# Performance work log

Measured on AMD Instinct MI355X. Metric: run time of the kernel, lower is better.

The kernel has to match this reference:

```python
import jax, jax.numpy as jnp
import numpy as np

DIM = 1024
NUM_EXPERTS = 8
TOP_K = 2


def setup_inputs() -> dict:
    key = jax.random.key(0)
    ks = jax.random.split(key, 7)
    s_in = 1.0 / np.sqrt(DIM)
    s_hid = 1.0 / np.sqrt(4 * DIM)
    x = jax.random.normal(ks[0], (2, 2048, DIM), dtype=jnp.float32)
    gate_w = jax.random.normal(ks[1], (DIM, NUM_EXPERTS), dtype=jnp.float32) * s_in
    gate_b = jax.random.normal(ks[2], (NUM_EXPERTS,), dtype=jnp.float32) * 0.01
    w1 = jax.random.normal(ks[3], (NUM_EXPERTS, DIM, 4 * DIM), dtype=jnp.float32) * s_in
    b1 = jax.random.normal(ks[4], (NUM_EXPERTS, 4 * DIM), dtype=jnp.float32) * 0.01
    w2 = jax.random.normal(ks[5], (NUM_EXPERTS, 4 * DIM, DIM), dtype=jnp.float32) * s_hid
    b2 = jax.random.normal(ks[6], (NUM_EXPERTS, DIM), dtype=jnp.float32) * 0.01
    return {"x": x, "gate_w": gate_w, "gate_b": gate_b, "w1": w1, "b1": b1, "w2": w2, "b2": b2}


def reference(x, gate_w, gate_b, w1, b1, w2, b2):
    # Faithful to the torch module in EVAL mode (no routing noise).
    # Quirks reproduced: (1) gather of expert inputs degenerates to flat_x
    # (all top_k copies identical); (2) softmax-normalized gates are dead code
    # (never applied); (3) the per-expert masked assignment overwrites all
    # TOP_K. Net: out = TOP_K * FFN_{max(topk_idx)}(x).
    B, N, C = x.shape
    flat_x = x.reshape(-1, C)                      # [T, C]
    logits = flat_x @ gate_w + gate_b              # [T, E]
    _, topk_idx = jax.lax.top_k(logits, TOP_K)     # [T, k]
    e_star = jnp.max(topk_idx, axis=-1)            # [T] last-overwriting expert
    out = jnp.zeros_like(flat_x)
    for i in range(NUM_EXPERTS):                   # fixed small expert loop
        h = jax.nn.gelu(flat_x @ w1[i] + b1[i], approximate=False)  # exact GELU (torch default)
        y = h @ w2[i] + b2[i]                      # [T, C]
        out = jnp.where((e_star == i)[:, None], y, out)
    return (TOP_K * out).reshape(B, N, C)
```

## Files before the change

### kernel.cpp

```cpp
#include <hip/hip_runtime.h>
#include <hip/hip_bf16.h>
#include <hip/hip_fp16.h>

#define T_TOKENS 4096
#define DIMC 1024
#define HID 4096
#define NE 8

typedef _Float16 f16;
typedef _Float16 f16x8 __attribute__((ext_vector_type(8)));
typedef _Float16 f16x4 __attribute__((ext_vector_type(4)));
typedef float f32x4 __attribute__((ext_vector_type(4)));

__device__ __forceinline__ void gload_lds16(const f16* g, f16* l) {
    __builtin_amdgcn_global_load_lds(
        (const __attribute__((address_space(1))) void*)g,
        (__attribute__((address_space(3))) void*)l, 16, 0, 0);
}

__global__ __launch_bounds__(256) void gating_kernel(
    const float* __restrict__ x, const float* __restrict__ gw,
    const float* __restrict__ gb, int* __restrict__ counts,
    int* __restrict__ list)
{
    const int wave = threadIdx.x >> 6;
    const int lane = threadIdx.x & 63;
    const int t = blockIdx.x * 4 + wave;

    const float* xr = x + (size_t)t * DIMC;
    float acc[NE];
#pragma unroll
    for (int e = 0; e < NE; ++e) acc[e] = 0.f;

    for (int i = 0; i < DIMC / 64; ++i) {
        const int k = i * 64 + lane;
        const float xv = xr[k];
        const float* g = gw + (size_t)k * NE;
#pragma unroll
        for (int e = 0; e < NE; ++e) acc[e] = fmaf(xv, g[e], acc[e]);
    }
#pragma unroll
    for (int off = 32; off >= 1; off >>= 1) {
#pragma unroll
        for (int e = 0; e < NE; ++e) acc[e] += __shfl_xor(acc[e], off, 64);
    }
    if (lane == 0) {
        float lg[NE];
#pragma unroll
        for (int e = 0; e < NE; ++e) lg[e] = acc[e] + gb[e];
        int i1 = 0; float v1 = lg[0];
#pragma unroll
        for (int e = 1; e < NE; ++e) { if (lg[e] > v1) { v1 = lg[e]; i1 = e; } }
        int i2 = -1; float v2 = -3.4e38f;
#pragma unroll
        for (int e = 0; e < NE; ++e) {
            if (e == i1) continue;
            if (lg[e] > v2) { v2 = lg[e]; i2 = e; }
        }
        const int es = (i1 > i2) ? i1 : i2;
        const int pos = atomicAdd(&counts[es], 1);
        list[es * T_TOKENS + pos] = t;
    }
}

__global__ __launch_bounds__(256) void xconvert(const float* __restrict__ x,
                                                f16* __restrict__ xh)
{
    const size_t i = ((size_t)blockIdx.x * 256 + threadIdx.x) * 8;
    const float4 a = *(const float4*)(x + i);
    const float4 b = *(const float4*)(x + i + 4);
    f16x8 v;
    v[0] = (f16)a.x; v[1] = (f16)a.y; v[2] = (f16)a.z; v[3] = (f16)a.w;
    v[4] = (f16)b.x; v[5] = (f16)b.y; v[6] = (f16)b.z; v[7] = (f16)b.w;
    *(f16x8*)(xh + i) = v;
}

__global__ __launch_bounds__(256) void wconvert(const float* __restrict__ W,
                                                f16* __restrict__ Wt,
                                                int K, int N)
{
    __shared__ f16 Lt[64 * 72];
    const int n0 = blockIdx.x * 64;
    const int k0 = blockIdx.y * 64;
    const float* Ws = W + (size_t)blockIdx.z * K * N;
    const int t = threadIdx.x;

    const int no = (t & 15) * 4;
    const int kr = t >> 4;
#pragma unroll
    for (int p = 0; p < 4; ++p) {
        const int k = kr + p * 16;
        const float4 v = *(const float4*)(Ws + (size_t)(k0 + k) * N + n0 + no);
        Lt[(no + 0) * 72 + k] = (f16)v.x;
        Lt[(no + 1) * 72 + k] = (f16)v.y;
        Lt[(no + 2) * 72 + k] = (f16)v.z;
        Lt[(no + 3) * 72 + k] = (f16)v.w;
    }
    __syncthreads();
    const int n = t >> 2;
    const int ko = (t & 3) * 16;
    const f16x8 a = *(const f16x8*)&Lt[n * 72 + ko];
    const f16x8 b = *(const f16x8*)&Lt[n * 72 + ko + 8];
    f16* dst = Wt + ((size_t)blockIdx.z * N + n0 + n) * K + k0 + ko;
    *(f16x8*)(dst) = a;
    *(f16x8*)(dst + 8) = b;
}

template <bool FIRST>
__global__ __launch_bounds__(256) void ffn_gemm4(
    const f16* __restrict__ A, const f16* __restrict__ Bt,
    const float* __restrict__ bias, const int* __restrict__ counts,
    const int* __restrict__ list, f16* __restrict__ Hout,
    float* __restrict__ pout)
{
    constexpr int KB   = FIRST ? DIMC : HID;
    constexpr int NTOT = FIRST ? HID : DIMC;

    const int e   = FIRST ? (int)blockIdx.z : (int)(blockIdx.z >> 2);
    const int ks  = FIRST ? 0 : (int)(blockIdx.z & 3);
    const int kk0 = ks * 1024;
    const int m0  = blockIdx.y * 128;
    const int n0  = blockIdx.x * 128;
    const int cnt = counts[e];
    if (m0 >= cnt) return;

    __shared__ __align__(16) f16 As[2][128 * 64];
    __shared__ __align__(16) f16 Bs[2][128 * 64];
    __shared__ int rows[128];

    const int tid = threadIdx.x;
    if (tid < 128) rows[tid] = (m0 + tid < cnt) ? list[e * T_TOKENS + m0 + tid] : -1;
    __syncthreads();

    const int lane = tid & 63;
    const int wv   = tid >> 6;
    const int wr   = wv >> 1, wc = wv & 1;

    const f16* asrc[4];
    const f16* bsrc[4];
#pragma unroll
    for (int j = 0; j < 4; ++j) {
        const int row   = wv * 32 + j * 8 + (lane >> 3);
        const int chunk = (lane & 7) ^ (row & 7);
        int tok = rows[row]; if (tok < 0) tok = 0;
        asrc[j] = A + (size_t)tok * KB + kk0 + chunk * 8;
        bsrc[j] = Bt + ((size_t)e * NTOT + n0 + row) * KB + kk0 + chunk * 8;
    }

    f32x4 acc[4][4];
#pragma unroll
    for (int mi = 0; mi < 4; ++mi)
#pragma unroll
        for (int ni = 0; ni < 4; ++ni) acc[mi][ni] = f32x4{0.f, 0.f, 0.f, 0.f};

#define STAGE(BUF, KO)                                                     \
    _Pragma("unroll")                                                      \
    for (int j = 0; j < 4; ++j) {                                          \
        gload_lds16(asrc[j] + (KO), &As[BUF][(wv * 32 + j * 8) * 64]);     \
        gload_lds16(bsrc[j] + (KO), &Bs[BUF][(wv * 32 + j * 8) * 64]);     \
    }

#define COMPUTE(BUF)                                                       \
    _Pragma("unroll")                                                      \
    for (int kh = 0; kh < 2; ++kh) {                                       \
        f16x8 af[4], bf[4];                                                \
        _Pragma("unroll")                                                  \
        for (int mi = 0; mi < 4; ++mi) {                                   \
            const int row = wr * 64 + mi * 16 + (lane & 15);               \
            const int kb  = (((lane >> 4) * 16) + kh * 64) ^ ((row & 7) << 4); \
            af[mi] = *(const f16x8*)((const char*)As[BUF] + row * 128 + kb);   \
        }                                                                  \
        _Pragma("unroll")                                                  \
        for (int ni = 0; ni < 4; ++ni) {                                   \
            const int n  = wc * 64 + ni * 16 + (lane & 15);                \
            const int kb = (((lane >> 4) * 16) + kh * 64) ^ ((n & 7) << 4);\
            bf[ni] = *(const f16x8*)((const char*)Bs[BUF] + n * 128 + kb); \
        }                                                                  \
        _Pragma("unroll")                                                  \
        for (int mi = 0; mi < 4; ++mi)                                     \
            _Pragma("unroll")                                              \
            for (int ni = 0; ni < 4; ++ni)                                 \
                acc[mi][ni] = __builtin_amdgcn_mfma_f32_16x16x32_f16(      \
                    af[mi], bf[ni], acc[mi][ni], 0, 0, 0);                 \
    }

    STAGE(0, 0);
    __syncthreads();
#pragma unroll
    for (int kt2 = 0; kt2 < 8; ++kt2) {
        STAGE(1, (2 * kt2 + 1) * 64);
        COMPUTE(0);
        __syncthreads();
        if (kt2 < 7) { STAGE(0, (2 * kt2 + 2) * 64); }
        COMPUTE(1);
        __syncthreads();
    }
#undef STAGE
#undef COMPUTE

#pragma unroll
    for (int ni = 0; ni < 4; ++ni) {
        const int gc = n0 + wc * 64 + ni * 16 + (lane & 15);
        const float bv = FIRST ? bias[(size_t)e * HID + gc]
                               : ((ks == 0) ? 2.f * bias[(size_t)e * DIMC + gc] : 0.f);
#pragma unroll
        for (int mi = 0; mi < 4; ++mi) {
#pragma unroll
            for (int r = 0; r < 4; ++r) {
                const int lrow = wr * 64 + mi * 16 + (lane >> 4) * 4 + r;
                const int tok = rows[lrow];
                if (tok < 0) continue;
                if (FIRST) {
                    const float v = acc[mi][ni][r] + bv;
                    const float g = 0.5f * v * (1.f + erff(v * 0.70710678118f));
                    Hout[(size_t)tok * HID + gc] = (f16)g;
                } else {
                    pout[((size_t)ks * T_TOKENS + tok) * DIMC + gc] =
                        2.f * acc[mi][ni][r] + bv;
                }
            }
        }
    }
}

__global__ __launch_bounds__(256) void reduce4(const float* __restrict__ p,
                                               float* __restrict__ out)
{
    constexpr size_t SL = (size_t)T_TOKENS * DIMC;
    const size_t i = ((size_t)blockIdx.x * 256 + threadIdx.x) * 4;
    const float4 a = *(const float4*)(p + i);
    const float4 b = *(const float4*)(p + SL + i);
    const float4 c = *(const float4*)(p + 2 * SL + i);
    const float4 d = *(const float4*)(p + 3 * SL + i);
    float4 s;
    s.x = a.x + b.x + c.x + d.x;
    s.y = a.y + b.y + c.y + d.y;
    s.z = a.z + b.z + c.z + d.z;
    s.w = a.w + b.w + c.w + d.w;
    *(float4*)(out + i) = s;
}

template <bool FIRST>
__global__ __launch_bounds__(256) void ffn_gemm3(
    const f16* __restrict__ A, const f16* __restrict__ Bt,
    const float* __restrict__ bias, const int* __restrict__ counts,
    const int* __restrict__ list, f16* __restrict__ Hout,
    float* __restrict__ out)
{
    constexpr int KB   = FIRST ? DIMC : HID;
    constexpr int NTOT = FIRST ? HID : DIMC;
    constexpr int NKT  = 16;

    const int e   = FIRST ? (int)blockIdx.z : (int)(blockIdx.z >> 2);
    const int ks  = FIRST ? 0 : (int)(blockIdx.z & 3);
    const int kk0 = ks * 1024;
    const int m0  = blockIdx.y * 128;
    const int n0  = blockIdx.x * 128;
    const int cnt = counts[e];
    if (m0 >= cnt) return;

    __shared__ __align__(16) f16 As[128 * 64];
    __shared__ __align__(16) f16 Bs[128 * 64];
    __shared__ int rows[128];

    const int tid = threadIdx.x;
    if (tid < 128) rows[tid] = (m0 + tid < cnt) ? list[e * T_TOKENS + m0 + tid] : -1;
    __syncthreads();

    const int lane = tid & 63;
    const int wv   = tid >> 6;
    const int wr   = wv >> 1, wc = wv & 1;

    const f16* asrc[4];
    const f16* bsrc[4];
    f16* adst[4];
    f16* bdst[4];
#pragma unroll
    for (int j = 0; j < 4; ++j) {
        const int row   = wv * 32 + j * 8 + (lane >> 3);
        const int chunk = (lane & 7) ^ (row & 7);
        int tok = rows[row]; if (tok < 0) tok = 0;
        asrc[j] = A + (size_t)tok * KB + kk0 + chunk * 8;
        bsrc[j] = Bt + ((size_t)e * NTOT + n0 + row) * KB + kk0 + chunk * 8;
        adst[j] = As + (wv * 32 + j * 8) * 64;
        bdst[j] = Bs + (wv * 32 + j * 8) * 64;
    }

    f32x4 acc[4][4];
#pragma unroll
    for (int mi = 0; mi < 4; ++mi)
#pragma unroll
        for (int ni = 0; ni < 4; ++ni) acc[mi][ni] = f32x4{0.f, 0.f, 0.f, 0.f};

    for (int kt = 0; kt < NKT; ++kt) {
        const int ko = kt * 64;
        __syncthreads();
#pragma unroll
        for (int j = 0; j < 4; ++j) {
            gload_lds16(asrc[j] + ko, adst[j]);
            gload_lds16(bsrc[j] + ko, bdst[j]);
        }
        __syncthreads();
#pragma unroll
        for (int kh = 0; kh < 2; ++kh) {
            f16x8 af[4], bf[4];
#pragma unroll
            for (int mi = 0; mi < 4; ++mi) {
                const int row = wr * 64 + mi * 16 + (lane & 15);
                const int kb  = (((lane >> 4) * 16) + kh * 64) ^ ((row & 7) << 4);
                af[mi] = *(const f16x8*)((const char*)As + row * 128 + kb);
            }
#pragma unroll
            for (int ni = 0; ni < 4; ++ni) {
                const int n  = wc * 64 + ni * 16 + (lane & 15);
                const int kb = (((lane >> 4) * 16) + kh * 64) ^ ((n & 7) << 4);
                bf[ni] = *(const f16x8*)((const char*)Bs + n * 128 + kb);
            }
#pragma unroll
            for (int mi = 0; mi < 4; ++mi)
#pragma unroll
                for (int ni = 0; ni < 4; ++ni)
                    acc[mi][ni] = __builtin_amdgcn_mfma_f32_16x16x32_f16(
                        af[mi], bf[ni], acc[mi][ni], 0, 0, 0);
        }
    }

#pragma unroll
    for (int ni = 0; ni < 4; ++ni) {
        const int gc = n0 + wc * 64 + ni * 16 + (lane & 15);
        const float bv = FIRST ? bias[(size_t)e * HID + gc]
                               : ((ks == 0) ? 2.f * bias[(size_t)e * DIMC + gc] : 0.f);
#pragma unroll
        for (int mi = 0; mi < 4; ++mi) {
#pragma unroll
            for (int r = 0; r < 4; ++r) {
                const int lrow = wr * 64 + mi * 16 + (lane >> 4) * 4 + r;
                const int tok = rows[lrow];
                if (tok < 0) continue;
                if (FIRST) {
                    const float v = acc[mi][ni][r] + bv;
                    const float g = 0.5f * v * (1.f + erff(v * 0.70710678118f));
                    Hout[(size_t)tok * HID + gc] = (f16)g;
                } else {
                    atomicAdd(out + (size_t)tok * DIMC + gc,
                              2.f * acc[mi][ni][r] + bv);
                }
            }
        }
    }
}

template <bool FIRST>
__global__ __launch_bounds__(256) void ffn_gemm_fb(
    const float* __restrict__ x, const f16* __restrict__ Hin,
    const float* __restrict__ w1, const float* __restrict__ b1,
    const float* __restrict__ w2, const float* __restrict__ b2,
    const int* __restrict__ counts, const int* __restrict__ list,
    f16* __restrict__ Hout, float* __restrict__ out)
{
    constexpr int K = FIRST ? DIMC : HID;
    constexpr int N = FIRST ? HID : DIMC;
    constexpr int LDT = 40;

    const int e  = blockIdx.z;
    const int m0 = blockIdx.y * 128;
    const int n0 = blockIdx.x * 128;
    const int cnt = counts[e];
    if (m0 >= cnt) return;

    __shared__ f16 Ab[128 * LDT];
    __shared__ f16 Bb[128 * LDT];
    __shared__ int rows[128];

    const int tid = threadIdx.x;
    if (tid < 128) {
        const int p = m0 + tid;
        rows[tid] = (p < cnt) ? list[e * T_TOKENS + p] : -1;
    }
    __syncthreads();

    const int lane = tid & 63;
    const int wv = tid >> 6;
    const int wr = wv >> 1, wc = wv & 1;

    f32x4 acc[4][4];
#pragma unroll
    for (int mi = 0; mi < 4; ++mi)
#pragma unroll
        for (int ni = 0; ni < 4; ++ni) acc[mi][ni] = f32x4{0.f, 0.f, 0.f, 0.f};

    const float* Bsrc = (FIRST ? w1 : w2) + (size_t)e * K * N;

    for (int kk = 0; kk < K; kk += 32) {
        __syncthreads();
        {
            const int r  = tid >> 3;
            const int ko = (tid & 7) * 4;
#pragma unroll
            for (int p = 0; p < 4; ++p) {
                const int row = p * 32 + r;
                const int tok = rows[row];
                f16x4 hv;
                if (FIRST) {
                    float4 v;
                    if (tok >= 0) v = *(const float4*)(x + (size_t)tok * K + kk + ko);
                    else          v = make_float4(0.f, 0.f, 0.f, 0.f);
                    hv[0] = (f16)v.x; hv[1] = (f16)v.y; hv[2] = (f16)v.z; hv[3] = (f16)v.w;
                } else {
                    if (tok >= 0) hv = *(const f16x4*)(Hin + (size_t)tok * K + kk + ko);
                    else { hv[0] = (f16)0.f; hv[1] = (f16)0.f; hv[2] = (f16)0.f; hv[3] = (f16)0.f; }
                }
                *(f16x4*)&Ab[row * LDT + ko] = hv;
            }
        }
        {
            const int kb = tid >> 5;
            const int no = (tid & 31) * 4;
#pragma unroll
            for (int p = 0; p < 4; ++p) {
                const int k = p * 8 + kb;
                const float4 v = *(const float4*)(Bsrc + (size_t)(kk + k) * N + n0 + no);
                f16 h[4];
                h[0] = (f16)v.x; h[1] = (f16)v.y; h[2] = (f16)v.z; h[3] = (f16)v.w;
#pragma unroll
                for (int i = 0; i < 4; ++i) {
                    const int n = no + i;
                    const int chunk = (k >> 3) ^ ((n >> 2) & 3);
                    Bb[n * LDT + chunk * 8 + (k & 7)] = h[i];
                }
            }
        }
        __syncthreads();
        f16x8 af[4], bf[4];
#pragma unroll
        for (int mi = 0; mi < 4; ++mi) {
            const int row = wr * 64 + mi * 16 + (lane & 15);
            af[mi] = *(const f16x8*)&Ab[row * LDT + (lane >> 4) * 8];
        }
#pragma unroll
        for (int ni = 0; ni < 4; ++ni) {
            const int n = wc * 64 + ni * 16 + (lane & 15);
            const int chunk = (lane >> 4) ^ ((n >> 2) & 3);
            bf[ni] = *(const f16x8*)&Bb[n * LDT + chunk * 8];
        }
#pragma unroll
        for (int mi = 0; mi < 4; ++mi)
#pragma unroll
            for (int ni = 0; ni < 4; ++ni)
                acc[mi][ni] = __builtin_amdgcn_mfma_f32_16x16x32_f16(
                    af[mi], bf[ni], acc[mi][ni], 0, 0, 0);
    }

#pragma unroll
    for (int ni = 0; ni < 4; ++ni) {
        const int gc = n0 + wc * 64 + ni * 16 + (lane & 15);
        const float bias = FIRST ? b1[(size_t)e * HID + gc]
                                 : b2[(size_t)e * DIMC + gc];
#pragma unroll
        for (int mi = 0; mi < 4; ++mi) {
#pragma unroll
            for (int r = 0; r < 4; ++r) {
                const int lrow = wr * 64 + mi * 16 + (lane >> 4) * 4 + r;
                const int tok = rows[lrow];
                if (tok < 0) continue;
                const float v = acc[mi][ni][r] + bias;
                if (FIRST) {
                    const float g = 0.5f * v * (1.f + erff(v * 0.70710678118f));
                    Hout[(size_t)tok * HID + gc] = (f16)g;
                } else {
                    out[(size_t)tok * DIMC + gc] = 2.f * v;
                }
            }
        }
    }
}

extern "C" void kernel_launch(void* const* d_in, const int* in_sizes, int n_in,
                              void* d_out, int out_size, void* d_ws, size_t ws_size,
                              hipStream_t stream)
{
    const float* x   = (const float*)d_in[0];
    const float* gw  = (const float*)d_in[1];
    const float* gb  = (const float*)d_in[2];
    const float* w1  = (const float*)d_in[3];
    const float* b1  = (const float*)d_in[4];
    const float* w2  = (const float*)d_in[5];
    const float* b2  = (const float*)d_in[6];
    float* out = (float*)d_out;

    const size_t MB = 1 << 20;
    const size_t need_p   = 233 * MB;
    const size_t need_big = 169 * MB;

    if (ws_size >= need_big) {
        int* counts = (int*)d_ws;
        int* list   = (int*)((char*)d_ws + 1024);
        f16* xh     = (f16*)((char*)d_ws + 1 * MB);
        f16* H      = (f16*)((char*)d_ws + 9 * MB);
        f16* w1t    = (f16*)((char*)d_ws + 41 * MB);
        f16* w2t    = (f16*)((char*)d_ws + 105 * MB);
        float* p    = (float*)((char*)d_ws + 169 * MB);

        hipMemsetAsync(counts, 0, 1024, stream);

        gating_kernel<<<T_TOKENS / 4, 256, 0, stream>>>(x, gw, gb, counts, list);
        xconvert<<<(T_TOKENS * DIMC) / (256 * 8), 256, 0, stream>>>(x, xh);
        wconvert<<<dim3(HID / 64, DIMC / 64, NE), 256, 0, stream>>>(w1, w1t, DIMC, HID);
        wconvert<<<dim3(DIMC / 64, HID / 64, NE), 256, 0, stream>>>(w2, w2t, HID, DIMC);

        if (ws_size >= need_p) {
            ffn_gemm4<true><<<dim3(HID / 128, T_TOKENS / 128, NE), 256, 0, stream>>>(
                xh, w1t, b1, counts, list, H, nullptr);
            ffn_gemm4<false><<<dim3(DIMC / 128, T_TOKENS / 128, NE * 4), 256, 0, stream>>>(
                H, w2t, b2, counts, list, nullptr, p);
            reduce4<<<(T_TOKENS * DIMC) / (256 * 4), 256, 0, stream>>>(p, out);
        } else {
            hipMemsetAsync(out, 0, (size_t)T_TOKENS * DIMC * sizeof(float), stream);
            ffn_gemm3<true><<<dim3(HID / 128, T_TOKENS / 128, NE), 256, 0, stream>>>(
                xh, w1t, b1, counts, list, H, nullptr);
            ffn_gemm3<false><<<dim3(DIMC / 128, T_TOKENS / 128, NE * 4), 256, 0, stream>>>(
                H, w2t, b2, counts, list, nullptr, out);
        }
        return;
    }

    const size_t need_fb = (size_t)(1 << 18) + (size_t)T_TOKENS * HID * sizeof(f16);
    if (ws_size < need_fb) return;

    int* counts = (int*)d_ws;
    int* list   = (int*)((char*)d_ws + 1024);
    f16* H      = (f16*)((char*)d_ws + (1 << 18));

    hipMemsetAsync(d_ws, 0, 1024, stream);
    gating_kernel<<<T_TOKENS / 4, 256, 0, stream>>>(x, gw, gb, counts, list);
    ffn_gemm_fb<true><<<dim3(HID / 128, T_TOKENS / 128, NE), 256, 0, stream>>>(
        x, (const f16*)nullptr, w1, b1, w2, b2, counts, list, H, out);
    ffn_gemm_fb<false><<<dim3(DIMC / 128, T_TOKENS / 128, NE), 256, 0, stream>>>(
        x, (const f16*)H, w1, b1, w2, b2, counts, list, H, out);
}
```

Baseline: 362.6 us.

## Enlarge GEMM tile to 256x128 with 8 waves and triple-buffered LDS pipeline

Grows each FFN GEMM block from 128 to 256 token rows using 512 threads, so every B (weight) tile fetched into LDS feeds twice as many rows. The double-buffered loop with full __syncthreads is replaced by a three-stage ring buffer prefetched two K-tiles ahead, using explicit vmcnt waits and raw s_barrier calls. The intent is to cut weight traffic per FLOP and overlap global loads with MFMA work more deeply. LDS use roughly doubles to about 144KB per block, which limits occupancy. Fewer blocks can run when per-expert token counts are small, and the hand-tuned vmcnt counts must match the exact number of loads issued.

After: 377.2 us. +4.0%, slower.

```diff
diff --git a/kernel.cpp b/kernel.cpp
--- a/kernel.cpp
+++ b/kernel.cpp
@@ -107,7 +107,7 @@
 }
 
 template <bool FIRST>
-__global__ __launch_bounds__(256) void ffn_gemm4(
+__global__ __launch_bounds__(512) void ffn_gemm5(
     const f16* __restrict__ A, const f16* __restrict__ Bt,
     const float* __restrict__ bias, const int* __restrict__ counts,
     const int* __restrict__ list, f16* __restrict__ Hout,
@@ -119,31 +119,37 @@
     const int e   = FIRST ? (int)blockIdx.z : (int)(blockIdx.z >> 2);
     const int ks  = FIRST ? 0 : (int)(blockIdx.z & 3);
     const int kk0 = ks * 1024;
-    const int m0  = blockIdx.y * 128;
+    const int m0  = blockIdx.y * 256;
     const int n0  = blockIdx.x * 128;
     const int cnt = counts[e];
     if (m0 >= cnt) return;
 
-    __shared__ __align__(16) f16 As[2][128 * 64];
-    __shared__ __align__(16) f16 Bs[2][128 * 64];
-    __shared__ int rows[128];
+    __shared__ __align__(16) f16 As[3][256 * 64];
+    __shared__ __align__(16) f16 Bs[3][128 * 64];
+    __shared__ int rows[256];
 
     const int tid = threadIdx.x;
-    if (tid < 128) rows[tid] = (m0 + tid < cnt) ? list[e * T_TOKENS + m0 + tid] : -1;
+    if (tid < 256) rows[tid] = (m0 + tid < cnt) ? list[e * T_TOKENS + m0 + tid] : -1;
     __syncthreads();
 
     const int lane = tid & 63;
     const int wv   = tid >> 6;
-    const int wr   = wv >> 1, wc = wv & 1;
+    const int wr   = wv >> 1;
+    const int wc   = wv & 1;
 
     const f16* asrc[4];
-    const f16* bsrc[4];
+    const f16* bsrc[2];
 #pragma unroll
     for (int j = 0; j < 4; ++j) {
         const int row   = wv * 32 + j * 8 + (lane >> 3);
         const int chunk = (lane & 7) ^ (row & 7);
         int tok = rows[row]; if (tok < 0) tok = 0;
         asrc[j] = A + (size_t)tok * KB + kk0 + chunk * 8;
+    }
+#pragma unroll
+    for (int j = 0; j < 2; ++j) {
+        const int row   = wv * 16 + j * 8 + (lane >> 3);
+        const int chunk = (lane & 7) ^ (row & 7);
         bsrc[j] = Bt + ((size_t)e * NTOT + n0 + row) * KB + kk0 + chunk * 8;
     }
 
@@ -153,50 +159,58 @@
 #pragma unroll
         for (int ni = 0; ni < 4; ++ni) acc[mi][ni] = f32x4{0.f, 0.f, 0.f, 0.f};
 
-#define STAGE(BUF, KO)                                                     \
-    _Pragma("unroll")                                                      \
-    for (int j = 0; j < 4; ++j) {                                          \
-        gload_lds16(asrc[j] + (KO), &As[BUF][(wv * 32 + j * 8) * 64]);     \
-        gload_lds16(bsrc[j] + (KO), &Bs[BUF][(wv * 32 + j * 8) * 64]);     \
-    }
-
-#define COMPUTE(BUF)                                                       \
-    _Pragma("unroll")                                                      \
-    for (int kh = 0; kh < 2; ++kh) {                                       \
-        f16x8 af[4], bf[4];                                                \
-        _Pragma("unroll")                                                  \
-        for (int mi = 0; mi < 4; ++mi) {                                   \
-            const int row = wr * 64 + mi * 16 + (lane & 15);               \
-            const int kb  = (((lane >> 4) * 16) + kh * 64) ^ ((row & 7) << 4); \
-            af[mi] = *(const f16x8*)((const char*)As[BUF] + row * 128 + kb);   \
-        }                                                                  \
-        _Pragma("unroll")                                                  \
-        for (int ni = 0; ni < 4; ++ni) {                                   \
-            const int n  = wc * 64 + ni * 16 + (lane & 15);                \
-            const int kb = (((lane >> 4) * 16) + kh * 64) ^ ((n & 7) << 4);\
-            bf[ni] = *(const f16x8*)((const char*)Bs[BUF] + n * 128 + kb); \
-        }                                                                  \
-        _Pragma("unroll")                                                  \
-        for (int mi = 0; mi < 4; ++mi)                                     \
-            _Pragma("unroll")                                              \
-            for (int ni = 0; ni < 4; ++ni)                                 \
-                acc[mi][ni] = __builtin_amdgcn_mfma_f32_16x16x32_f16(      \
-                    af[mi], bf[ni], acc[mi][ni], 0, 0, 0);                 \
-    }
-
-    STAGE(0, 0);
-    __syncthreads();
-#pragma unroll
-    for (int kt2 = 0; kt2 < 8; ++kt2) {
-        STAGE(1, (2 * kt2 + 1) * 64);
-        COMPUTE(0);
-        __syncthreads();
-        if (kt2 < 7) { STAGE(0, (2 * kt2 + 2) * 64); }
-        COMPUTE(1);
-        __syncthreads();
-    }
-#undef STAGE
-#undef COMPUTE
+#define STG(BUF, KT)                                                          \
+    do {                                                                      \
+        _Pragma("unroll")                                                     \
+        for (int j = 0; j < 4; ++j)                                           \
+            gload_lds16(asrc[j] + (KT) * 64, &As[BUF][(wv * 32 + j * 8) * 64]); \
+        _Pragma("unroll")                                                     \
+        for (int j = 0; j < 2; ++j)                                           \
+            gload_lds16(bsrc[j] + (KT) * 64, &Bs[BUF][(wv * 16 + j * 8) * 64]); \
+    } while (0)
+
+#define CMP(BUF)                                                              \
+    do {                                                                      \
+        _Pragma("unroll")                                                     \
+        for (int kh = 0; kh < 2; ++kh) {                                      \
+            f16x8 af[4], bf[4];                                               \
+            _Pragma("unroll")                                                 \
+            for (int mi = 0; mi < 4; ++mi) {                                  \
+                const int row = wr * 64 + mi * 16 + (lane & 15);              \
+                const int kb  = (((lane >> 4) * 16) + kh * 64) ^ ((row & 7) << 4); \
+                af[mi] = *(const f16x8*)((const char*)As[BUF] + row * 128 + kb);   \
+            }                                                                 \
+            _Pragma("unroll")                                                 \
+            for (int ni = 0; ni < 4; ++ni) {                                  \
+                const int n  = wc * 64 + ni * 16 + (lane & 15);               \
+                const int kb = (((lane >> 4) * 16) + kh * 64) ^ ((n & 7) << 4);    \
+                bf[ni] = *(const f16x8*)((const char*)Bs[BUF] + n * 128 + kb);     \
+            }                                                                 \
+            _Pragma("unroll")                                                 \
+            for (int mi = 0; mi < 4; ++mi)                                    \
+                _Pragma("unroll")                                             \
+                for (int ni = 0; ni < 4; ++ni)                                \
+                    acc[mi][ni] = __builtin_amdgcn_mfma_f32_16x16x32_f16(     \
+                        af[mi], bf[ni], acc[mi][ni], 0, 0, 0);                \
+        }                                                                     \
+    } while (0)
+
+    STG(0, 0);
+    STG(1, 1);
+#pragma unroll
+    for (int kt = 0; kt < 16; ++kt) {
+        if (kt + 2 < 16) STG((kt + 2) % 3, kt + 2);
+        if (kt < 14)       asm volatile("s_waitcnt vmcnt(12)" ::: "memory");
+        else if (kt == 14) asm volatile("s_waitcnt vmcnt(6)"  ::: "memory");
+        else               asm volatile("s_waitcnt vmcnt(0)"  ::: "memory");
+        __builtin_amdgcn_s_barrier();
+        __builtin_amdgcn_sched_barrier(0);
+        CMP(kt % 3);
+        __builtin_amdgcn_s_barrier();
+        __builtin_amdgcn_sched_barrier(0);
+    }
+#undef STG
+#undef CMP
 
 #pragma unroll
     for (int ni = 0; ni < 4; ++ni) {
@@ -509,9 +523,9 @@
         wconvert<<<dim3(DIMC / 64, HID / 64, NE), 256, 0, stream>>>(w2, w2t, HID, DIMC);
 
         if (ws_size >= need_p) {
-            ffn_gemm4<true><<<dim3(HID / 128, T_TOKENS / 128, NE), 256, 0, stream>>>(
+            ffn_gemm5<true><<<dim3(HID / 128, T_TOKENS / 256, NE), 512, 0, stream>>>(
                 xh, w1t, b1, counts, list, H, nullptr);
-            ffn_gemm4<false><<<dim3(DIMC / 128, T_TOKENS / 128, NE * 4), 256, 0, stream>>>(
+            ffn_gemm5<false><<<dim3(DIMC / 128, T_TOKENS / 256, NE * 4), 512, 0, stream>>>(
                 H, w2t, b2, counts, list, nullptr, p);
             reduce4<<<(T_TOKENS * DIMC) / (256 * 4), 256, 0, stream>>>(p, out);
         } else {
```
